# Kernel optimization log

Measured on AMD Instinct MI355X. Metric: run time of the kernel, lower is better.

## Reference

```python
import jax, jax.numpy as jnp
import numpy as np

D_MODEL = 2048
N_HEADS = 16
HEAD_DIM = D_MODEL // N_HEADS
B, T = 2, 2048


def setup_inputs() -> dict:
    key = jax.random.key(0)
    ks = jax.random.split(key, 7)
    s = 0.02
    return {
        "x": jax.random.normal(ks[0], (B, T, D_MODEL), dtype=jnp.float32),
        "w_qkv": jax.random.normal(ks[1], (D_MODEL, 3 * D_MODEL), dtype=jnp.float32) * s,
        "w_proj": jax.random.normal(ks[2], (D_MODEL, D_MODEL), dtype=jnp.float32) * s,
        "w_ff1": jax.random.normal(ks[3], (D_MODEL, 4 * D_MODEL), dtype=jnp.float32) * s,
        "b_ff1": jnp.zeros((4 * D_MODEL,), dtype=jnp.float32),
        "w_ff2": jax.random.normal(ks[4], (4 * D_MODEL, D_MODEL), dtype=jnp.float32) * s,
        "b_ff2": jnp.zeros((D_MODEL,), dtype=jnp.float32),
    }


def reference(x, w_qkv, w_proj, w_ff1, b_ff1, w_ff2, b_ff2):
    Bs, Ts, C = x.shape
    H, hd = N_HEADS, HEAD_DIM
    # fused qkv projection
    qkv = jnp.einsum("btc,cd->btd", x, w_qkv)
    q, k, v = jnp.split(qkv, 3, axis=-1)
    # (B, T, C) -> (B, H, T, hd)
    q = q.reshape(Bs, Ts, H, hd).transpose(0, 2, 1, 3)
    k = k.reshape(Bs, Ts, H, hd).transpose(0, 2, 1, 3)
    v = v.reshape(Bs, Ts, H, hd).transpose(0, 2, 1, 3)
    # paged KV write + gather round-trip (empty cache, n_kv_head == n_heads)
    # is the identity on k, v; attention is causal SDPA over the full cache.
    scale = 1.0 / jnp.sqrt(jnp.asarray(hd, dtype=x.dtype))
    scores = jnp.einsum("bhqd,bhkd->bhqk", q, k) * scale
    causal = jnp.tril(jnp.ones((Ts, Ts), dtype=bool))
    scores = jnp.where(causal, scores, jnp.finfo(scores.dtype).min)
    attn = jax.nn.softmax(scores, axis=-1)
    out = jnp.einsum("bhqk,bhkd->bhqd", attn, v)  # (B, H, T, hd)
    out = out.transpose(0, 2, 1, 3).reshape(Bs, Ts, C)
    attn_out = jnp.einsum("btc,cd->btd", out, w_proj)
    # feed-forward with exact GELU (torch nn.GELU default)
    h = jax.nn.gelu(jnp.einsum("btc,cf->btf", x, w_ff1) + b_ff1, approximate=False)
    ff_out = jnp.einsum("btf,fc->btc", h, w_ff2) + b_ff2
    return x + attn_out + ff_out
```

## Files before the change

kernel.cpp:

```cpp
#include <hip/hip_runtime.h>
#include <hip/hip_bf16.h>
#include <cmath>

typedef __bf16 bf16x8 __attribute__((ext_vector_type(8)));
typedef float f32x4 __attribute__((ext_vector_type(4)));
typedef unsigned short u16;
typedef unsigned int u32;

#define DEV __device__ __forceinline__

static constexpr int BB = 2;
static constexpr int T = 2048;
static constexpr int DM = 2048;
static constexpr int NH = 16;
static constexpr int HD = 128;
static constexpr int FF = 8192;
static constexpr int M = BB * T;
static constexpr int NQKV = 3 * DM;

DEV u16 f2b(float f) {
  u32 u = __builtin_bit_cast(u32, f);
  u = (u + 0x7FFFu + ((u >> 16) & 1u)) >> 16;
  return (u16)u;
}
DEV float b2f(u16 h) {
  u32 u = ((u32)h) << 16;
  return __builtin_bit_cast(float, u);
}

DEV void gload16(const u16* g, const u16* l) {
  __builtin_amdgcn_global_load_lds(
      (const __attribute__((address_space(1))) void*)(uintptr_t)g,
      (__attribute__((address_space(3))) void*)(unsigned)(uintptr_t)l,
      16, 0, 0);
}


__global__ void cvt_f32_to_bf16(const float* __restrict__ in, u16* __restrict__ out, int n4) {
  int i = blockIdx.x * blockDim.x + threadIdx.x;
  if (i >= n4) return;
  float4 v = reinterpret_cast<const float4*>(in)[i];
  ushort4 o;
  o.x = f2b(v.x); o.y = f2b(v.y); o.z = f2b(v.z); o.w = f2b(v.w);
  reinterpret_cast<ushort4*>(out)[i] = o;
}

__global__ void transpose_cvt(const float* __restrict__ W, u16* __restrict__ Wt, int K, int N) {
  __shared__ float tile[32][33];
  int nb = blockIdx.x * 32, kb = blockIdx.y * 32;
  int r = threadIdx.x >> 3;
  int c4 = (threadIdx.x & 7) * 4;
  float4 v = *reinterpret_cast<const float4*>(&W[(size_t)(kb + r) * N + nb + c4]);
  tile[r][c4] = v.x; tile[r][c4 + 1] = v.y; tile[r][c4 + 2] = v.z; tile[r][c4 + 3] = v.w;
  __syncthreads();
  ushort4 o;
  o.x = f2b(tile[c4][r]);     o.y = f2b(tile[c4 + 1][r]);
  o.z = f2b(tile[c4 + 2][r]); o.w = f2b(tile[c4 + 3][r]);
  *reinterpret_cast<ushort4*>(&Wt[(size_t)(nb + r) * K + kb + c4]) = o;
}

template <int EPI>
__global__ __launch_bounds__(512, 2) void gemm8(
    const u16* __restrict__ A, const u16* __restrict__ Bt, int Ndim, int K, int gx,
    u16* __restrict__ out_bf, const float* __restrict__ bias) {
  __shared__ __align__(16) u16 lds[2 * 32768];
  const int t = threadIdx.x;
  const int nwg = gridDim.x, cpx = nwg >> 3;
  const int wg = (blockIdx.x & 7) * cpx + (blockIdx.x >> 3);
  const int m0 = (wg / gx) * 256, n0 = (wg % gx) * 256;
  const int wave = t >> 6, lane = t & 63;
  const int wm = wave >> 2, wn = wave & 3;
  const int lr = lane & 15, lk = lane >> 4;

  const int srow = t >> 3;
  const int sc8 = ((t & 7) ^ (srow & 7)) * 8;
  const u16* gA = &A[(size_t)(m0 + srow) * K + sc8];
  const u16* gB = &Bt[(size_t)(n0 + srow) * K + sc8];
  const int wls = wave * 512;

  u16* buf0 = lds;
  u16* buf1 = lds + 32768;

#define STAGE_A(buf, h, kt)                                                      \
  {                                                                              \
    gload16(gA + (size_t)((h) * 128) * K + (kt) * 64, (buf) + (h) * 8192 + wls); \
    gload16(gA + (size_t)((h) * 128 + 64) * K + (kt) * 64,                       \
            (buf) + (h) * 8192 + 4096 + wls);                                    \
  }
#define STAGE_B(buf, h, kt)                                                      \
  {                                                                              \
    gload16(gB + (size_t)((h) * 128) * K + (kt) * 64,                            \
            (buf) + 16384 + (h) * 8192 + wls);                                   \
    gload16(gB + (size_t)((h) * 128 + 64) * K + (kt) * 64,                       \
            (buf) + 16384 + (h) * 8192 + 4096 + wls);                            \
  }
#define PH_PRE                          \
  __builtin_amdgcn_sched_barrier(0);    \
  __builtin_amdgcn_s_barrier();         \
  __builtin_amdgcn_sched_barrier(0);    \
  __builtin_amdgcn_s_setprio(1);
#define PH_POST                         \
  __builtin_amdgcn_s_setprio(0);        \
  __builtin_amdgcn_sched_barrier(0);    \
  __builtin_amdgcn_s_barrier();         \
  __builtin_amdgcn_sched_barrier(0);

  const int NT = K >> 6;

  STAGE_A(buf0, 0, 0); STAGE_A(buf0, 1, 0);
  STAGE_B(buf0, 0, 0); STAGE_B(buf0, 1, 0);
  STAGE_A(buf1, 0, 1); STAGE_B(buf1, 0, 1);
  __builtin_amdgcn_sched_barrier(0);
  asm volatile("s_waitcnt vmcnt(4)" ::: "memory");
  __builtin_amdgcn_s_barrier();
  __builtin_amdgcn_sched_barrier(0);

  f32x4 acc[8][4] = {};
  const int aBase = (wm * 128 + lr) * 64;
  const int bBase = 16384 + (wn * 64 + lr) * 64;
  const int c0 = (lk ^ (lr & 7)) * 8;
  const int c1 = ((4 + lk) ^ (lr & 7)) * 8;

  u16* cur = buf0;
  u16* alt = buf1;
  bf16x8 af[4][2], bq0[2][2], bq1[2][2];

  for (int kt = 0; kt < NT; ++kt) {
#pragma unroll
    for (int i = 0; i < 4; ++i) {
      af[i][0] = *(const bf16x8*)&cur[aBase + i * 1024 + c0];
      af[i][1] = *(const bf16x8*)&cur[aBase + i * 1024 + c1];
    }
#pragma unroll
    for (int j = 0; j < 2; ++j) {
      bq0[j][0] = *(const bf16x8*)&cur[bBase + j * 1024 + c0];
      bq0[j][1] = *(const bf16x8*)&cur[bBase + j * 1024 + c1];
    }
    if (kt + 1 < NT) STAGE_A(alt, 1, kt + 1);
    PH_PRE;
#pragma unroll
    for (int i = 0; i < 4; ++i)
#pragma unroll
      for (int j = 0; j < 2; ++j)
#pragma unroll
        for (int kk = 0; kk < 2; ++kk)
          acc[i][j] = __builtin_amdgcn_mfma_f32_16x16x32_bf16(af[i][kk], bq0[j][kk], acc[i][j], 0, 0, 0);
    PH_POST;
#pragma unroll
    for (int j = 0; j < 2; ++j) {
      bq1[j][0] = *(const bf16x8*)&cur[bBase + (2 + j) * 1024 + c0];
      bq1[j][1] = *(const bf16x8*)&cur[bBase + (2 + j) * 1024 + c1];
    }
    if (kt + 1 < NT) STAGE_B(alt, 1, kt + 1);
    PH_PRE;
#pragma unroll
    for (int i = 0; i < 4; ++i)
#pragma unroll
      for (int j = 0; j < 2; ++j)
#pragma unroll
        for (int kk = 0; kk < 2; ++kk)
          acc[i][2 + j] = __builtin_amdgcn_mfma_f32_16x16x32_bf16(af[i][kk], bq1[j][kk], acc[i][2 + j], 0, 0, 0);
    PH_POST;
#pragma unroll
    for (int i = 0; i < 4; ++i) {
      af[i][0] = *(const bf16x8*)&cur[aBase + (4 + i) * 1024 + c0];
      af[i][1] = *(const bf16x8*)&cur[aBase + (4 + i) * 1024 + c1];
    }
    if (kt + 2 < NT) STAGE_A(cur, 0, kt + 2);
    PH_PRE;
#pragma unroll
    for (int i = 0; i < 4; ++i)
#pragma unroll
      for (int j = 0; j < 2; ++j)
#pragma unroll
        for (int kk = 0; kk < 2; ++kk)
          acc[4 + i][2 + j] = __builtin_amdgcn_mfma_f32_16x16x32_bf16(af[i][kk], bq1[j][kk], acc[4 + i][2 + j], 0, 0, 0);
    PH_POST;
    if (kt + 2 < NT) STAGE_B(cur, 0, kt + 2);
    PH_PRE;
#pragma unroll
    for (int i = 0; i < 4; ++i)
#pragma unroll
      for (int j = 0; j < 2; ++j)
#pragma unroll
        for (int kk = 0; kk < 2; ++kk)
          acc[4 + i][j] = __builtin_amdgcn_mfma_f32_16x16x32_bf16(af[i][kk], bq0[j][kk], acc[4 + i][j], 0, 0, 0);
    __builtin_amdgcn_s_setprio(0);
    __builtin_amdgcn_sched_barrier(0);
    if (kt + 2 < NT)      asm volatile("s_waitcnt vmcnt(4)" ::: "memory");
    else if (kt + 1 < NT) asm volatile("s_waitcnt vmcnt(0)" ::: "memory");
    __builtin_amdgcn_s_barrier();
    __builtin_amdgcn_sched_barrier(0);
    u16* tmp = cur; cur = alt; alt = tmp;
  }
#undef STAGE_A
#undef STAGE_B
#undef PH_PRE
#undef PH_POST

#pragma unroll
  for (int i = 0; i < 8; ++i) {
#pragma unroll
    for (int j = 0; j < 4; ++j) {
#pragma unroll
      for (int r = 0; r < 4; ++r) {
        int gr = m0 + wm * 128 + i * 16 + (lane >> 4) * 4 + r;
        int gc = n0 + wn * 64 + j * 16 + (lane & 15);
        float v = acc[i][j][r];
        if constexpr (EPI == 0) {
          int part = gc >> 11, cc = gc & 2047;
          int head = cc >> 7, d = cc & 127;
          int b = gr >> 11, tt = gr & 2047;
          out_bf[(size_t)part * M * DM + (((size_t)(b * NH + head) * T + tt) * HD + d)] = f2b(v);
        } else {
          v += bias[gc];
          float u = v * (v * v * 0.044715f + 1.0f) * 0.7978845608028654f;
          float e = exp2f(u * 2.885390081777927f);
          float th = 1.0f - 2.0f / (e + 1.0f);
          v = 0.5f * v * (1.0f + th);
          out_bf[(size_t)gr * Ndim + gc] = f2b(v);
        }
      }
    }
  }
}

template <int EPI>
__global__ __launch_bounds__(512, 4) void gemm_bf16(
    const u16* __restrict__ A, const u16* __restrict__ Bt, int Ndim, int K, int gx,
    u16* __restrict__ out_bf, float* __restrict__ out_f32,
    const float* __restrict__ bias,
    const float* __restrict__ resid_f32, const u16* __restrict__ resid_bf) {
  __shared__ __align__(16) u16 lds[3 * (256 + 128) * 32];
  const int t = threadIdx.x;
  const int nwg = gridDim.x, cpx = nwg >> 3;
  const int wg = (blockIdx.x & 7) * cpx + (blockIdx.x >> 3);
  const int m0 = (wg / gx) * 256, n0 = (wg % gx) * 128;
  const int wave = t >> 6, lane = t & 63;
  const int wm = wave >> 1, wn = wave & 1;
  const int lr = lane & 15, lk = lane >> 4;

  u16* cA = lds;                   u16* cB = lds + 8192;
  u16* nA = lds + 12288;           u16* nB = lds + 12288 + 8192;
  u16* sA = lds + 2 * 12288;       u16* sB = lds + 2 * 12288 + 8192;

  const int sk = ((lane & 3) ^ ((lane >> 3) & 3)) * 8;
  const u16* gA0 = &A[(size_t)(m0 + wave * 16 + (lane >> 2)) * K + sk];
  const u16* gA1 = gA0 + (size_t)128 * K;
  const u16* gB0 = &Bt[(size_t)(n0 + wave * 16 + (lane >> 2)) * K + sk];

  const int wbase = wave * 512;

  auto stage = [&](u16* dA, u16* dB) {
    gload16(gA0, dA + wbase);
    gload16(gA1, dA + 4096 + wbase);
    gload16(gB0, dB + wbase);
    gA0 += 32; gA1 += 32; gB0 += 32;
  };

  const int NT = K >> 5;

  stage(cA, cB);
  stage(nA, nB);
  __builtin_amdgcn_sched_barrier(0);
  asm volatile("s_waitcnt vmcnt(3)" ::: "memory");
  __builtin_amdgcn_s_barrier();
  __builtin_amdgcn_sched_barrier(0);

  f32x4 acc[4][4] = {};
  const int rcol = (lk ^ ((lr >> 1) & 3)) * 8;

  for (int kt = 0; kt < NT; ++kt) {
    if (kt + 2 < NT) stage(sA, sB);
    bf16x8 af[4], bfr[4];
#pragma unroll
    for (int i = 0; i < 4; ++i) {
      af[i]  = *reinterpret_cast<const bf16x8*>(&cA[(wm * 64 + i * 16 + lr) * 32 + rcol]);
      bfr[i] = *reinterpret_cast<const bf16x8*>(&cB[(wn * 64 + i * 16 + lr) * 32 + rcol]);
    }
#pragma unroll
    for (int i = 0; i < 4; ++i)
#pragma unroll
      for (int j = 0; j < 4; ++j)
        acc[i][j] = __builtin_amdgcn_mfma_f32_16x16x32_bf16(af[i], bfr[j], acc[i][j], 0, 0, 0);
    if (kt + 1 < NT) {
      __builtin_amdgcn_sched_barrier(0);
      if (kt + 2 < NT) asm volatile("s_waitcnt vmcnt(3)" ::: "memory");
      else             asm volatile("s_waitcnt vmcnt(0)" ::: "memory");
      __builtin_amdgcn_s_barrier();
      __builtin_amdgcn_sched_barrier(0);
      u16* tA = cA; u16* tB = cB;
      cA = nA; cB = nB; nA = sA; nB = sB; sA = tA; sB = tB;
    }
  }

#pragma unroll
  for (int i = 0; i < 4; ++i) {
#pragma unroll
    for (int j = 0; j < 4; ++j) {
#pragma unroll
      for (int r = 0; r < 4; ++r) {
        int gr = m0 + wm * 64 + i * 16 + (lane >> 4) * 4 + r;
        int gc = n0 + wn * 64 + j * 16 + (lane & 15);
        float v = acc[i][j][r];
        if constexpr (EPI == 1) {
          out_bf[(size_t)gr * Ndim + gc] = f2b(v);
        } else if constexpr (EPI == 3) {
          v += bias[gc] + resid_f32[(size_t)gr * Ndim + gc] + b2f(resid_bf[(size_t)gr * Ndim + gc]);
          out_f32[(size_t)gr * Ndim + gc] = v;
        } else {
          int hh = gr >> 7, d = gr & 127;
          int b = gc >> 11, tt = gc & 2047;
          out_bf[((size_t)(b * NH + hh) * HD + d) * T + tt] = f2b(v);
        }
      }
    }
  }
}

__global__ __launch_bounds__(256) void attn_fwd(
    const u16* __restrict__ qg, const u16* __restrict__ kg,
    const u16* __restrict__ vt, u16* __restrict__ outg) {
  __shared__ __align__(16) u16 lK[2][64 * 128];
  __shared__ __align__(16) u16 lVt[2][128 * 64];
  __shared__ __align__(16) u16 lP[4][16 * 72];
  const int t = threadIdx.x;
  const int qi = gridDim.x - 1 - blockIdx.x;
  const int bh = blockIdx.y;
  const int wv = t >> 6, lane = t & 63;
  const int lc = lane & 15, lg = lane >> 4;
  const size_t base = (size_t)bh * T * HD;
  const size_t vbase = (size_t)bh * HD * T;
  const int q0 = qi * 64;

  bf16x8 qf[4];
#pragma unroll
  for (int kk = 0; kk < 4; ++kk)
    qf[kk] = *reinterpret_cast<const bf16x8*>(
        &qg[base + (size_t)(q0 + wv * 16 + lc) * HD + kk * 32 + lg * 8]);

  f32x4 oacc[8] = {};
  float mrow[4], lrow[4];
#pragma unroll
  for (int r = 0; r < 4; ++r) { mrow[r] = -INFINITY; lrow[r] = 0.f; }

  auto stageKV = [&](int kt, int b) {
#pragma unroll
    for (int h = 0; h < 4; ++h) {
      int c = t + h * 256;
      int row = c >> 4;
      int sb = ((c & 15) * 16) ^ ((row & 7) << 4);
      gload16(&kg[base + (size_t)(kt * 64 + row) * HD + (sb >> 1)],
              (const u16*)((const char*)lK[b] + (h * 256 + wv * 64) * 16));
    }
#pragma unroll
    for (int h = 0; h < 4; ++h) {
      int c = t + h * 256;
      int row = c >> 3;
      int sb = ((c & 7) * 16) ^ ((row & 7) << 4);
      gload16(&vt[vbase + (size_t)row * T + kt * 64 + (sb >> 1)],
              (const u16*)((const char*)lVt[b] + (h * 256 + wv * 64) * 16));
    }
  };

  const float scaleL = 0.08838834764831845f * 1.4426950408889634f;
  const int ntiles = qi + 1;

  stageKV(0, 0);
  __builtin_amdgcn_sched_barrier(0);
  asm volatile("s_waitcnt vmcnt(0)" ::: "memory");
  __builtin_amdgcn_s_barrier();
  __builtin_amdgcn_sched_barrier(0);

  for (int kt = 0; kt < ntiles; ++kt) {
    const int cb = kt & 1;
    if (kt + 1 < ntiles) stageKV(kt + 1, cb ^ 1);
    const u16* lKc = lK[cb];
    const u16* lVc = lVt[cb];

    f32x4 s[4] = {};
    __builtin_amdgcn_s_setprio(1);
#pragma unroll
    for (int nf = 0; nf < 4; ++nf) {
      int krow = nf * 16 + lc;
#pragma unroll
      for (int kk = 0; kk < 4; ++kk) {
        int dbyte = kk * 64 + lg * 16;
        bf16x8 kf = *reinterpret_cast<const bf16x8*>(
            reinterpret_cast<const char*>(lKc) + krow * 256 + (dbyte ^ ((krow & 7) << 4)));
        s[nf] = __builtin_amdgcn_mfma_f32_16x16x32_bf16(qf[kk], kf, s[nf], 0, 0, 0);
      }
    }
    __builtin_amdgcn_s_setprio(0);

    float rmax[4];
#pragma unroll
    for (int r = 0; r < 4; ++r) rmax[r] = -INFINITY;
#pragma unroll
    for (int nf = 0; nf < 4; ++nf) {
      int col = kt * 64 + nf * 16 + lc;
#pragma unroll
      for (int r = 0; r < 4; ++r) {
        int row = q0 + wv * 16 + lg * 4 + r;
        float sv = s[nf][r] * scaleL;
        if (col > row) sv = -INFINITY;
        s[nf][r] = sv;
        rmax[r] = fmaxf(rmax[r], sv);
      }
    }
#pragma unroll
    for (int mk = 1; mk < 16; mk <<= 1)
#pragma unroll
      for (int r = 0; r < 4; ++r)
        rmax[r] = fmaxf(rmax[r], __shfl_xor(rmax[r], mk));

    int need = 0;
#pragma unroll
    for (int r = 0; r < 4; ++r) need |= (rmax[r] > mrow[r] + 11.5f) ? 1 : 0;
    if (__any(need)) {
      float corr[4];
#pragma unroll
      for (int r = 0; r < 4; ++r) {
        float mnew = fmaxf(mrow[r], rmax[r]);
        corr[r] = exp2f(mrow[r] - mnew);
        mrow[r] = mnew;
        lrow[r] *= corr[r];
      }
#pragma unroll
      for (int dc = 0; dc < 8; ++dc)
#pragma unroll
        for (int r = 0; r < 4; ++r) oacc[dc][r] *= corr[r];
    }

#pragma unroll
    for (int nf = 0; nf < 4; ++nf) {
#pragma unroll
      for (int r = 0; r < 4; ++r) {
        float p = exp2f(s[nf][r] - mrow[r]);
        lrow[r] += p;
        lP[wv][(lg * 4 + r) * 72 + nf * 16 + lc] = f2b(p);
      }
    }
    bf16x8 pa[2];
#pragma unroll
    for (int kk = 0; kk < 2; ++kk)
      pa[kk] = *reinterpret_cast<const bf16x8*>(&lP[wv][lc * 72 + kk * 32 + lg * 8]);
    __builtin_amdgcn_s_setprio(1);
#pragma unroll
    for (int dc = 0; dc < 8; ++dc) {
#pragma unroll
      for (int kk = 0; kk < 2; ++kk) {
        int vrow = dc * 16 + lc;
        int off = (kk * 64 + lg * 16) ^ ((vrow & 7) << 4);
        bf16x8 vf = *reinterpret_cast<const bf16x8*>(
            reinterpret_cast<const char*>(lVc) + vrow * 128 + off);
        oacc[dc] = __builtin_amdgcn_mfma_f32_16x16x32_bf16(pa[kk], vf, oacc[dc], 0, 0, 0);
      }
    }
    __builtin_amdgcn_s_setprio(0);

    __builtin_amdgcn_sched_barrier(0);
    if (kt + 1 < ntiles) asm volatile("s_waitcnt vmcnt(0)" ::: "memory");
    __builtin_amdgcn_s_barrier();
    __builtin_amdgcn_sched_barrier(0);
  }

#pragma unroll
  for (int mk = 1; mk < 16; mk <<= 1)
#pragma unroll
    for (int r = 0; r < 4; ++r) lrow[r] += __shfl_xor(lrow[r], mk);

  const int b = bh >> 4, hh = bh & 15;
#pragma unroll
  for (int dc = 0; dc < 8; ++dc)
#pragma unroll
    for (int r = 0; r < 4; ++r) {
      int tt = q0 + wv * 16 + lg * 4 + r;
      int d = dc * 16 + lc;
      float o = oacc[dc][r] / lrow[r];
      outg[(size_t)(b * T + tt) * DM + hh * HD + d] = f2b(o);
    }
}


extern "C" void kernel_launch(void* const* d_in, const int* in_sizes, int n_in,
                              void* d_out, int out_size, void* d_ws, size_t ws_size,
                              hipStream_t stream) {
  const float* x      = (const float*)d_in[0];
  const float* w_qkv  = (const float*)d_in[1];
  const float* w_proj = (const float*)d_in[2];
  const float* w_ff1  = (const float*)d_in[3];
  const float* b_ff1  = (const float*)d_in[4];
  const float* w_ff2  = (const float*)d_in[5];
  const float* b_ff2  = (const float*)d_in[6];
  float* out = (float*)d_out;

  u16* ws = (u16*)d_ws;
  size_t o = 0;
  u16* x_bf      = ws + o; o += (size_t)M * DM;
  u16* wqkv_t    = ws + o; o += (size_t)NQKV * DM;
  u16* wproj_t   = ws + o; o += (size_t)DM * DM;
  u16* wff1_t    = ws + o; o += (size_t)FF * DM;
  u16* wff2_t    = ws + o; o += (size_t)DM * FF;
  u16* attn_proj = ws + o; o += (size_t)M * DM;
  u16* qbuf      = ws + o;
  u16* kbuf      = qbuf + (size_t)M * DM;
  u16* vtbuf     = kbuf + (size_t)M * DM;
  u16* attn_out  = vtbuf + (size_t)M * DM;
  u16* hbuf      = qbuf;

  cvt_f32_to_bf16<<<(M * DM / 4 + 255) / 256, 256, 0, stream>>>(x, x_bf, M * DM / 4);
  transpose_cvt<<<dim3(NQKV / 32, DM / 32), 256, 0, stream>>>(w_qkv, wqkv_t, DM, NQKV);
  transpose_cvt<<<dim3(DM / 32, DM / 32), 256, 0, stream>>>(w_proj, wproj_t, DM, DM);
  transpose_cvt<<<dim3(FF / 32, DM / 32), 256, 0, stream>>>(w_ff1, wff1_t, DM, FF);
  transpose_cvt<<<dim3(DM / 32, FF / 32), 256, 0, stream>>>(w_ff2, wff2_t, FF, DM);

  gemm8<0><<<256, 512, 0, stream>>>(x_bf, wqkv_t, 4096, DM, 16, qbuf, nullptr);

  gemm_bf16<4><<<256, 512, 0, stream>>>(
      wqkv_t + (size_t)4096 * DM, x_bf, M, DM, 32, vtbuf, nullptr, nullptr, nullptr, nullptr);

  attn_fwd<<<dim3(T / 64, BB * NH), 256, 0, stream>>>(qbuf, kbuf, vtbuf, attn_out);

  gemm_bf16<1><<<256, 512, 0, stream>>>(
      attn_out, wproj_t, DM, DM, 16, attn_proj, nullptr, nullptr, nullptr, nullptr);

  gemm8<2><<<512, 512, 0, stream>>>(x_bf, wff1_t, FF, DM, 32, hbuf, b_ff1);

  gemm_bf16<3><<<256, 512, 0, stream>>>(
      hbuf, wff2_t, DM, FF, 16, nullptr, out, b_ff2, x, attn_proj);
}
```

Measured before the change: 659.1 us.

## Split-K the FF2 GEMM on the 256x256 kernel with separate reduce epilogue

The final FF2 GEMM (K=8192) now runs on the larger-tile gemm8 kernel, split into two K halves across 256 workgroups. Each half writes fp32 partial sums into reused workspace buffers. A new elementwise kernel adds the partials, bias, residual x and attention projection. The aim is a more efficient tile with full CU occupancy, at the cost of extra fp32 partial-sum traffic and one more launch.

```diff
diff --git a/kernel.cpp b/kernel.cpp
--- a/kernel.cpp
+++ b/kernel.cpp
@@ -59,23 +59,43 @@
   *reinterpret_cast<ushort4*>(&Wt[(size_t)(nb + r) * K + kb + c4]) = o;
 }
 
+__global__ void ff2_reduce(const float* __restrict__ p0, const float* __restrict__ p1,
+                           const float* __restrict__ bias, const float* __restrict__ x,
+                           const u16* __restrict__ ap, float* __restrict__ out) {
+  int i = blockIdx.x * blockDim.x + threadIdx.x;
+  float4 a = reinterpret_cast<const float4*>(p0)[i];
+  float4 b = reinterpret_cast<const float4*>(p1)[i];
+  float4 xx = reinterpret_cast<const float4*>(x)[i];
+  float4 bi = reinterpret_cast<const float4*>(bias)[i & (DM / 4 - 1)];
+  ushort4 a4 = reinterpret_cast<const ushort4*>(ap)[i];
+  float4 o;
+  o.x = a.x + b.x + bi.x + xx.x + b2f(a4.x);
+  o.y = a.y + b.y + bi.y + xx.y + b2f(a4.y);
+  o.z = a.z + b.z + bi.z + xx.z + b2f(a4.z);
+  o.w = a.w + b.w + bi.w + xx.w + b2f(a4.w);
+  reinterpret_cast<float4*>(out)[i] = o;
+}
+
 template <int EPI>
 __global__ __launch_bounds__(512, 2) void gemm8(
-    const u16* __restrict__ A, const u16* __restrict__ Bt, int Ndim, int K, int gx,
-    u16* __restrict__ out_bf, const float* __restrict__ bias) {
+    const u16* __restrict__ A, const u16* __restrict__ Bt, int Ndim,
+    int Kstride, int Klen, int gx, int tpp,
+    u16* __restrict__ out_bf, float* __restrict__ p0, float* __restrict__ p1,
+    const float* __restrict__ bias) {
   __shared__ __align__(16) u16 lds[2 * 32768];
   const int t = threadIdx.x;
   const int nwg = gridDim.x, cpx = nwg >> 3;
   const int wg = (blockIdx.x & 7) * cpx + (blockIdx.x >> 3);
-  const int m0 = (wg / gx) * 256, n0 = (wg % gx) * 256;
+  const int part = wg / tpp, tid = wg % tpp;
+  const int m0 = (tid / gx) * 256, n0 = (tid % gx) * 256;
   const int wave = t >> 6, lane = t & 63;
   const int wm = wave >> 2, wn = wave & 3;
   const int lr = lane & 15, lk = lane >> 4;
 
   const int srow = t >> 3;
   const int sc8 = ((t & 7) ^ (srow & 7)) * 8;
-  const u16* gA = &A[(size_t)(m0 + srow) * K + sc8];
-  const u16* gB = &Bt[(size_t)(n0 + srow) * K + sc8];
+  const u16* gA = &A[(size_t)(m0 + srow) * Kstride + (size_t)part * Klen + sc8];
+  const u16* gB = &Bt[(size_t)(n0 + srow) * Kstride + (size_t)part * Klen + sc8];
   const int wls = wave * 512;
 
   u16* buf0 = lds;
@@ -83,15 +103,16 @@
 
 #define STAGE_A(buf, h, kt)                                                      \
   {                                                                              \
-    gload16(gA + (size_t)((h) * 128) * K + (kt) * 64, (buf) + (h) * 8192 + wls); \
-    gload16(gA + (size_t)((h) * 128 + 64) * K + (kt) * 64,                       \
+    gload16(gA + (size_t)((h) * 128) * Kstride + (kt) * 64,                      \
+            (buf) + (h) * 8192 + wls);                                           \
+    gload16(gA + (size_t)((h) * 128 + 64) * Kstride + (kt) * 64,                 \
             (buf) + (h) * 8192 + 4096 + wls);                                    \
   }
 #define STAGE_B(buf, h, kt)                                                      \
   {                                                                              \
-    gload16(gB + (size_t)((h) * 128) * K + (kt) * 64,                            \
+    gload16(gB + (size_t)((h) * 128) * Kstride + (kt) * 64,                      \
             (buf) + 16384 + (h) * 8192 + wls);                                   \
-    gload16(gB + (size_t)((h) * 128 + 64) * K + (kt) * 64,                       \
+    gload16(gB + (size_t)((h) * 128 + 64) * Kstride + (kt) * 64,                 \
             (buf) + 16384 + (h) * 8192 + 4096 + wls);                            \
   }
 #define PH_PRE                          \
@@ -105,7 +126,7 @@
   __builtin_amdgcn_s_barrier();         \
   __builtin_amdgcn_sched_barrier(0);
 
-  const int NT = K >> 6;
+  const int NT = Klen >> 6;
 
   STAGE_A(buf0, 0, 0); STAGE_A(buf0, 1, 0);
   STAGE_B(buf0, 0, 0); STAGE_B(buf0, 1, 0);
@@ -198,6 +219,7 @@
 #undef PH_PRE
 #undef PH_POST
 
+  float* pout = (part == 0) ? p0 : p1;
 #pragma unroll
   for (int i = 0; i < 8; ++i) {
 #pragma unroll
@@ -208,17 +230,19 @@
         int gc = n0 + wn * 64 + j * 16 + (lane & 15);
         float v = acc[i][j][r];
         if constexpr (EPI == 0) {
-          int part = gc >> 11, cc = gc & 2047;
+          int part_ = gc >> 11, cc = gc & 2047;
           int head = cc >> 7, d = cc & 127;
           int b = gr >> 11, tt = gr & 2047;
-          out_bf[(size_t)part * M * DM + (((size_t)(b * NH + head) * T + tt) * HD + d)] = f2b(v);
-        } else {
+          out_bf[(size_t)part_ * M * DM + (((size_t)(b * NH + head) * T + tt) * HD + d)] = f2b(v);
+        } else if constexpr (EPI == 2) {
           v += bias[gc];
           float u = v * (v * v * 0.044715f + 1.0f) * 0.7978845608028654f;
           float e = exp2f(u * 2.885390081777927f);
           float th = 1.0f - 2.0f / (e + 1.0f);
           v = 0.5f * v * (1.0f + th);
           out_bf[(size_t)gr * Ndim + gc] = f2b(v);
+        } else {
+          pout[(size_t)gr * Ndim + gc] = v;
         }
       }
     }
@@ -509,13 +533,17 @@
   u16* attn_out  = vtbuf + (size_t)M * DM;
   u16* hbuf      = qbuf;
 
+  float* p0 = (float*)ws;
+  float* p1 = (float*)wff1_t;
+
   cvt_f32_to_bf16<<<(M * DM / 4 + 255) / 256, 256, 0, stream>>>(x, x_bf, M * DM / 4);
   transpose_cvt<<<dim3(NQKV / 32, DM / 32), 256, 0, stream>>>(w_qkv, wqkv_t, DM, NQKV);
   transpose_cvt<<<dim3(DM / 32, DM / 32), 256, 0, stream>>>(w_proj, wproj_t, DM, DM);
   transpose_cvt<<<dim3(FF / 32, DM / 32), 256, 0, stream>>>(w_ff1, wff1_t, DM, FF);
   transpose_cvt<<<dim3(DM / 32, FF / 32), 256, 0, stream>>>(w_ff2, wff2_t, FF, DM);
 
-  gemm8<0><<<256, 512, 0, stream>>>(x_bf, wqkv_t, 4096, DM, 16, qbuf, nullptr);
+  gemm8<0><<<256, 512, 0, stream>>>(x_bf, wqkv_t, 4096, DM, DM, 16, 256,
+                                    qbuf, nullptr, nullptr, nullptr);
 
   gemm_bf16<4><<<256, 512, 0, stream>>>(
       wqkv_t + (size_t)4096 * DM, x_bf, M, DM, 32, vtbuf, nullptr, nullptr, nullptr, nullptr);
@@ -525,8 +553,11 @@
   gemm_bf16<1><<<256, 512, 0, stream>>>(
       attn_out, wproj_t, DM, DM, 16, attn_proj, nullptr, nullptr, nullptr, nullptr);
 
-  gemm8<2><<<512, 512, 0, stream>>>(x_bf, wff1_t, FF, DM, 32, hbuf, b_ff1);
-
-  gemm_bf16<3><<<256, 512, 0, stream>>>(
-      hbuf, wff2_t, DM, FF, 16, nullptr, out, b_ff2, x, attn_proj);
-}
+  gemm8<2><<<512, 512, 0, stream>>>(x_bf, wff1_t, FF, DM, DM, 32, 512,
+                                    hbuf, nullptr, nullptr, b_ff1);
+
+  gemm8<5><<<256, 512, 0, stream>>>(hbuf, wff2_t, DM, FF, 4096, 8, 128,
+                                    nullptr, p0, p1, nullptr);
+
+  ff2_reduce<<<M * DM / 4 / 256, 256, 0, stream>>>(p0, p1, b_ff2, x, attn_proj, out);
+}
```

After: 646.4 us. About the same (-1.9%).
